# Performance work log

Hardware: AMD Instinct MI355X
Metric: run time of the kernel (lower is better)

The kernel has to match this reference:

```python
import jax, jax.numpy as jnp
import numpy as np

B, N = 32, 200000          # images, flattened candidates per image (anchors*classes)
NUM_CLASSES = 21           # VOC-style class count for the label-offset trick
CONF_THR = 0.05            # cfg.PRED_CONF_THR
NMS_THR = 0.5              # cfg.PRED_NMS_THR
TOPK = 500                 # cfg.PRED_SELECT_TOPK
KEEP_MAX = 100             # cfg.PRED_NMS_KEEP


def setup_inputs() -> dict:
    key = jax.random.key(0)
    k1, k2, k3, k4 = jax.random.split(key, 4)
    pscores = jax.random.uniform(k1, (B, N), dtype=jnp.float32)
    # well-formed ltrb boxes in [0,1]: right>left, bottom>top
    xy1 = jax.random.uniform(k2, (B, N, 2), dtype=jnp.float32) * 0.8
    wh = jax.random.uniform(k3, (B, N, 2), dtype=jnp.float32) * 0.2 + 0.01
    pboxes = jnp.concatenate([xy1, xy1 + wh], axis=-1)
    plabels = jax.random.randint(k4, (B, N), 0, NUM_CLASSES)
    return {"pscores": pscores, "pboxes": pboxes, "plabels": plabels}


def _box_iou(a, b):
    # a: [K,4], b: [K,4] ltrb -> [K,K] pairwise IoU (torchvision convention)
    lt = jnp.maximum(a[:, None, :2], b[None, :, :2])
    rb = jnp.minimum(a[:, None, 2:], b[None, :, 2:])
    wh = jnp.clip(rb - lt, 0.0)
    inter = wh[..., 0] * wh[..., 1]
    area_a = (a[:, 2] - a[:, 0]) * (a[:, 3] - a[:, 1])
    area_b = (b[:, 2] - b[:, 0]) * (b[:, 3] - b[:, 1])
    return inter / (area_a[:, None] + area_b[None, :] - inter)


def _greedy_nms(iou_mat, valid, thr):
    # candidates are pre-sorted by score descending (lax.top_k output order)
    K = valid.shape[0]
    idxs = jnp.arange(K)

    def body(keep, i):
        suppressed = jnp.any(keep & (iou_mat[i] > thr) & (idxs < i))
        k = valid[i] & (~suppressed)
        return keep.at[i].set(k), None

    keep, _ = jax.lax.scan(body, jnp.zeros((K,), dtype=bool), idxs)
    return keep


def reference(pscores, pboxes, plabels):
    # ---- threshold + top-k pre-selection (mask_pos AND mask_topk) ----
    scores_k, idx = jax.lax.top_k(pscores, TOPK)          # [B,K] sorted desc
    valid = scores_k > CONF_THR                           # equivalent to mask_pos & mask_topk
    bidx = jnp.arange(B)[:, None]
    boxes_k = pboxes[bidx, idx]                           # [B,K,4]
    labels_k = plabels[bidx, idx]                         # [B,K]

    # ---- multi-class NMS via label offset trick (batched_nms) ----
    max_coord = jnp.max(jnp.where(valid[..., None], boxes_k, 0.0), axis=(1, 2))  # [B]
    offsets = labels_k.astype(boxes_k.dtype) * (max_coord[:, None] + 1.0)
    boxes_nms = boxes_k + offsets[..., None]              # [B,K,4]

    iou = jax.vmap(_box_iou)(boxes_nms, boxes_nms)        # [B,K,K]
    keep = jax.vmap(lambda m, v: _greedy_nms(m, v, NMS_THR))(iou, valid)  # [B,K] bool

    # ---- keep[:num_max] per batch ----
    rank = jnp.cumsum(keep.astype(jnp.int32), axis=1)
    keep = keep & (rank <= KEEP_MAX)

    # compact kept entries to front (jnp.argsort is stable -> score order preserved), pad to KEEP_MAX
    order = jnp.argsort(jnp.where(keep, 0, 1), axis=1)[:, :KEEP_MAX]       # [B,KEEP]
    out_valid = jnp.take_along_axis(keep, order, axis=1)                    # [B,KEEP]
    boxes2 = jnp.take_along_axis(boxes_k, order[..., None], axis=1) * out_valid[..., None]
    scores2 = jnp.take_along_axis(scores_k, order, axis=1) * out_valid
    labels2 = jnp.where(out_valid, jnp.take_along_axis(labels_k, order, axis=1), -1)
    ids_batch2 = jnp.where(out_valid, jnp.arange(B)[:, None], -1)
    return ids_batch2, boxes2, labels2, scores2, out_valid
```

## Files before the change

kernel.cpp:

```cpp
#include <hip/hip_runtime.h>
#include <stdint.h>

#pragma clang fp contract(off)

#define BB 32
#define NN 200000
#define N4 50000
#define KK 500
#define KEEPN 100
#define CONF 0.05f
#define NMSTHR 0.5f
#define SLICES 8
#define SLICE_F4 6250
#define LBINS 8192
#define LSHIFT 19
#define LOCAL_CAP 2048
#define OUT_CAP 576
#define M_CAP (SLICES * OUT_CAP)

typedef unsigned long long u64;


__device__ __forceinline__ unsigned int ordkey(float s) {
    unsigned int u = __float_as_uint(s);
    return (u & 0x80000000u) ? ~u : (u | 0x80000000u);
}

__global__ __launch_bounds__(1024) void select_kernel(const float4* __restrict__ ps4,
                                                      u64* __restrict__ cand,
                                                      unsigned int* __restrict__ cnts) {
    __shared__ unsigned int hist[LBINS];
    __shared__ u64 keys[LOCAL_CAP];
    __shared__ unsigned int h[256];
    __shared__ unsigned int wsum[16];
    __shared__ u64 s_prefix;
    __shared__ unsigned int s_t13, s_region, s_cntgt;
    __shared__ int s_lcnt, s_sc;

    const int b = blockIdx.y, x = blockIdx.x;
    const int tid = threadIdx.x, lane = tid & 63, wv = tid >> 6;
    const float4* p = ps4 + (size_t)b * N4 + (size_t)x * SLICE_F4;

    for (int i = tid; i < LBINS; i += 1024) hist[i] = 0;
    __syncthreads();
    for (int i = tid; i < SLICE_F4; i += 1024) {
        float4 v = p[i];
        atomicAdd(&hist[ordkey(v.x) >> LSHIFT], 1u);
        atomicAdd(&hist[ordkey(v.y) >> LSHIFT], 1u);
        atomicAdd(&hist[ordkey(v.z) >> LSHIFT], 1u);
        atomicAdd(&hist[ordkey(v.w) >> LSHIFT], 1u);
    }
    __syncthreads();

    unsigned int v8[8], tot = 0;
    for (int j = 0; j < 8; ++j) { v8[j] = hist[tid * 8 + j]; tot += v8[j]; }
    unsigned int sfx = tot;
    for (int off = 1; off < 64; off <<= 1) {
        unsigned int t2 = __shfl_down(sfx, off);
        sfx += (lane + off < 64) ? t2 : 0u;
    }
    if (lane == 0) wsum[wv] = sfx;
    __syncthreads();
    unsigned int wafter = 0;
    for (int w2 = wv + 1; w2 < 16; ++w2) wafter += wsum[w2];
    unsigned int sn = wafter + (sfx - tot);
    for (int j = 7; j >= 0; --j) {
        unsigned int s = sn + v8[j];
        if (s >= (unsigned)KK && sn < (unsigned)KK) s_t13 = (unsigned)(tid * 8 + j);
        sn = s;
    }
    if (tid == 0) s_lcnt = 0;
    __syncthreads();

    const unsigned int t13 = s_t13;
    const int ebase = x * (SLICE_F4 * 4);
    for (int i = tid; i < SLICE_F4; i += 1024) {
        float4 v = p[i];
        int n = ebase + (i << 2);
        unsigned int u;
        u = ordkey(v.x); if ((u >> LSHIFT) >= t13) { int pos = atomicAdd(&s_lcnt, 1);
            if (pos < LOCAL_CAP) keys[pos] = ((u64)u << 32) | (unsigned int)(~(unsigned int)(n)); }
        u = ordkey(v.y); if ((u >> LSHIFT) >= t13) { int pos = atomicAdd(&s_lcnt, 1);
            if (pos < LOCAL_CAP) keys[pos] = ((u64)u << 32) | (unsigned int)(~(unsigned int)(n + 1)); }
        u = ordkey(v.z); if ((u >> LSHIFT) >= t13) { int pos = atomicAdd(&s_lcnt, 1);
            if (pos < LOCAL_CAP) keys[pos] = ((u64)u << 32) | (unsigned int)(~(unsigned int)(n + 2)); }
        u = ordkey(v.w); if ((u >> LSHIFT) >= t13) { int pos = atomicAdd(&s_lcnt, 1);
            if (pos < LOCAL_CAP) keys[pos] = ((u64)u << 32) | (unsigned int)(~(unsigned int)(n + 3)); }
    }
    __syncthreads();
    int m = s_lcnt; if (m > LOCAL_CAP) m = LOCAL_CAP;

    u64 thr; int seln;
    if (m <= OUT_CAP) {
        thr = 0ULL; seln = m;
    } else {
        if (tid == 0) { s_prefix = 0ULL; s_cntgt = 0u; }
        __syncthreads();
        int shift = 56;
        for (; shift >= 0; shift -= 8) {
            if (tid < 256) h[tid] = 0u;
            __syncthreads();
            u64 pref = s_prefix;
            unsigned int cg = s_cntgt;
            for (int i = tid; i < m; i += 1024) {
                u64 k = keys[i];
                bool match = (shift == 56) || ((k >> (shift + 8)) == pref);
                if (match) atomicAdd(&h[(unsigned int)((k >> shift) & 0xFF)], 1u);
            }
            __syncthreads();
            if (wv == 0) {
                unsigned int b4[4]; unsigned int lt = 0;
                for (int j = 0; j < 4; ++j) { b4[j] = h[lane * 4 + j]; lt += b4[j]; }
                unsigned int sx = lt;
                for (int off = 1; off < 64; off <<= 1) {
                    unsigned int t2 = __shfl_down(sx, off);
                    sx += (lane + off < 64) ? t2 : 0u;
                }
                unsigned int after = sx - lt;
                unsigned int target = (unsigned)KK - cg;
                unsigned int sn2 = after;
                for (int j = 3; j >= 0; --j) {
                    unsigned int s = sn2 + b4[j];
                    if (s >= target && sn2 < target) {
                        unsigned int bin = (unsigned)(lane * 4 + j);
                        s_region = b4[j];
                        s_cntgt = cg + sn2;
                        s_prefix = (shift == 56) ? (u64)bin : ((pref << 8) | (u64)bin);
                    }
                    sn2 = s;
                }
            }
            __syncthreads();
            if (s_cntgt + s_region <= (unsigned)OUT_CAP) break;
        }
        if (shift < 0) shift = 0;
        thr = s_prefix << shift;
        seln = (int)(s_cntgt + s_region);
    }
    (void)seln;

    if (tid == 0) s_sc = 0;
    __syncthreads();
    u64* outslice = cand + (size_t)(b * SLICES + x) * OUT_CAP;
    for (int r0 = 0; r0 < LOCAL_CAP / 1024; ++r0) {
        int i = tid + r0 * 1024;
        u64 k = (i < m) ? keys[i] : 0ULL;
        bool pq = (i < m) && (k >= thr);
        u64 mb = __ballot(pq);
        int pre = __popcll(mb & ((1ULL << lane) - 1ULL));
        int tt = __popcll(mb);
        int base = 0;
        if (lane == 0 && tt > 0) base = atomicAdd(&s_sc, tt);
        base = __shfl(base, 0);
        if (pq && base + pre < OUT_CAP) outslice[base + pre] = k;
    }
    __syncthreads();
    if (tid == 0) {
        int c = s_sc; if (c > OUT_CAP) c = OUT_CAP;
        cnts[b * SLICES + x] = (unsigned)c;
    }
}

__global__ __launch_bounds__(1024) void final_kernel(const float* __restrict__ pboxes,
                                                     const int* __restrict__ plabels,
                                                     const u64* __restrict__ cand,
                                                     const unsigned int* __restrict__ cnts,
                                                     float* __restrict__ out) {
    __shared__ u64 kbuf[M_CAP];
    __shared__ u64 sel[OUT_CAP];
    __shared__ float sboxes[KK * 4];
    __shared__ float sscore[KK];
    __shared__ int slabel[KK];
    __shared__ int clist[KK];
    __shared__ unsigned int h[256];
    __shared__ int ccnt[21], coff[22], cfill[21];
    __shared__ u64 validw[8];
    __shared__ int kept[KEEPN];
    __shared__ float wred[16];
    __shared__ int soff[SLICES + 1];
    __shared__ u64 s_prefix;
    __shared__ unsigned int s_region, s_cntgt;
    __shared__ int s_sc, s_nk;
    __shared__ float s_maxc;

    const int b = blockIdx.x;
    const int tid = threadIdx.x;
    const int lane = tid & 63;
    const int wv = tid >> 6;

    if (tid == 0) {
        int acc = 0;
        for (int s = 0; s < SLICES; ++s) {
            soff[s] = acc;
            int c = (int)cnts[b * SLICES + s];
            if (c > OUT_CAP) c = OUT_CAP;
            acc += c;
        }
        soff[SLICES] = acc;
    }
    __syncthreads();
    int m = soff[SLICES];
    for (int s = 0; s < SLICES; ++s) {
        int off = soff[s], len = soff[s + 1] - off;
        const u64* src = cand + (size_t)(b * SLICES + s) * OUT_CAP;
        for (int i = tid; i < len; i += 1024) kbuf[off + i] = src[i];
    }
    __syncthreads();

    u64 thr; int seln;
    if (m <= OUT_CAP) {
        thr = 0ULL; seln = m;
    } else {
        if (tid == 0) { s_prefix = 0ULL; s_cntgt = 0u; }
        __syncthreads();
        int shift = 56;
        for (; shift >= 0; shift -= 8) {
            if (tid < 256) h[tid] = 0u;
            __syncthreads();
            u64 pref = s_prefix;
            unsigned int cg = s_cntgt;
            for (int i = tid; i < m; i += 1024) {
                u64 k = kbuf[i];
                bool match = (shift == 56) || ((k >> (shift + 8)) == pref);
                if (match) atomicAdd(&h[(unsigned int)((k >> shift) & 0xFF)], 1u);
            }
            __syncthreads();
            if (wv == 0) {
                unsigned int b4[4]; unsigned int lt = 0;
                for (int j = 0; j < 4; ++j) { b4[j] = h[lane * 4 + j]; lt += b4[j]; }
                unsigned int sx = lt;
                for (int off = 1; off < 64; off <<= 1) {
                    unsigned int t2 = __shfl_down(sx, off);
                    sx += (lane + off < 64) ? t2 : 0u;
                }
                unsigned int after = sx - lt;
                unsigned int target = (unsigned)KK - cg;
                unsigned int sn2 = after;
                for (int j = 3; j >= 0; --j) {
                    unsigned int s = sn2 + b4[j];
                    if (s >= target && sn2 < target) {
                        unsigned int bin = (unsigned)(lane * 4 + j);
                        s_region = b4[j];
                        s_cntgt = cg + sn2;
                        s_prefix = (shift == 56) ? (u64)bin : ((pref << 8) | (u64)bin);
                    }
                    sn2 = s;
                }
            }
            __syncthreads();
            if (s_cntgt + s_region <= (unsigned)OUT_CAP) break;
        }
        if (shift < 0) shift = 0;
        thr = s_prefix << shift;
        seln = (int)(s_cntgt + s_region);
    }

    if (tid == 0) s_sc = 0;
    __syncthreads();
    for (int r0 = 0; r0 < (M_CAP + 1023) / 1024; ++r0) {
        int i = tid + r0 * 1024;
        u64 k = (i < m) ? kbuf[i] : 0ULL;
        bool pq = (i < m) && (k >= thr);
        u64 mb = __ballot(pq);
        int pre = __popcll(mb & ((1ULL << lane) - 1ULL));
        int tt = __popcll(mb);
        int base = 0;
        if (lane == 0 && tt > 0) base = atomicAdd(&s_sc, tt);
        base = __shfl(base, 0);
        if (pq) sel[base + pre] = k;
    }
    __syncthreads();

    u64 myk = (tid < seln) ? sel[tid] : 0ULL;
    int r = 0;
    if ((tid & ~63) < seln) {
        for (int base = 0; base < seln; base += 64) {
            int i2 = base + lane;
            u64 other = (i2 < seln) ? sel[i2] : 0ULL;
            unsigned int olo = (unsigned int)other, ohi = (unsigned int)(other >> 32);
            int lim = seln - base; if (lim > 64) lim = 64;
            for (int t2 = 0; t2 < lim; ++t2) {
                unsigned int blo = (unsigned int)__builtin_amdgcn_readlane((int)olo, t2);
                unsigned int bhi = (unsigned int)__builtin_amdgcn_readlane((int)ohi, t2);
                u64 o = ((u64)bhi << 32) | (u64)blo;
                r += (o > myk) ? 1 : 0;
            }
        }
    }
    __syncthreads();
    if (tid < seln && r < KK) sel[r] = myk;
    __syncthreads();

    float sc = -1.0f;
    if (tid < KK) {
        u64 key = sel[tid];
        unsigned int lo = (unsigned int)key;
        unsigned int hi = (unsigned int)(key >> 32);
        int idx = (int)(~lo);
        unsigned int bits = (hi & 0x80000000u) ? (hi & 0x7FFFFFFFu) : ~hi;
        sc = __uint_as_float(bits);
        sscore[tid] = sc;
        const float4 bx = *(const float4*)(pboxes + (((size_t)b * NN + (size_t)idx) << 2));
        sboxes[tid * 4 + 0] = bx.x; sboxes[tid * 4 + 1] = bx.y;
        sboxes[tid * 4 + 2] = bx.z; sboxes[tid * 4 + 3] = bx.w;
        slabel[tid] = plabels[(size_t)b * NN + idx];
    }
    __syncthreads();

    bool vq = (tid < KK) && (sc > CONF);
    u64 bm = __ballot(vq);
    if (lane == 0 && wv < 8) validw[wv] = bm;
    float lm = vq ? fmaxf(fmaxf(sboxes[tid * 4 + 0], sboxes[tid * 4 + 1]),
                          fmaxf(sboxes[tid * 4 + 2], sboxes[tid * 4 + 3])) : 0.0f;
    for (int off = 32; off > 0; off >>= 1) lm = fmaxf(lm, __shfl_down(lm, off));
    if (lane == 0) wred[wv] = lm;
    __syncthreads();
    if (tid < 64) {
        float x = (tid < 16) ? wred[tid] : 0.0f;
        for (int off = 8; off > 0; off >>= 1) x = fmaxf(x, __shfl_down(x, off));
        if (tid == 0) s_maxc = x;
    }
    if (tid < 21) { ccnt[tid] = 0; cfill[tid] = 0; }
    __syncthreads();
    if (tid < KK) atomicAdd(&ccnt[slabel[tid]], 1);
    __syncthreads();
    if (tid == 0) {
        int acc = 0;
        for (int c = 0; c < 21; ++c) { coff[c] = acc; acc += ccnt[c]; }
        coff[21] = acc;
    }
    __syncthreads();
    if (tid < KK) {
        int c = slabel[tid];
        int pos = atomicAdd(&cfill[c], 1);
        clist[coff[c] + pos] = tid;
    }
    for (int i = tid; i < KK * 8; i += 1024) kbuf[i] = 0ULL;
    __syncthreads();

    float ap1 = s_maxc + 1.0f;
    if (tid < KK) {
        int c = slabel[tid];
        int n = ccnt[c], base0 = coff[c];
        float aoff = (float)c * ap1;
        float a0 = sboxes[tid * 4 + 0] + aoff, a1 = sboxes[tid * 4 + 1] + aoff;
        float a2 = sboxes[tid * 4 + 2] + aoff, a3 = sboxes[tid * 4 + 3] + aoff;
        float areaA = (a2 - a0) * (a3 - a1);
        for (int q = 0; q < n; ++q) {
            int j = clist[base0 + q];
            float b0 = sboxes[j * 4 + 0] + aoff, b1f = sboxes[j * 4 + 1] + aoff;
            float b2f = sboxes[j * 4 + 2] + aoff, b3f = sboxes[j * 4 + 3] + aoff;
            float lt0 = fmaxf(a0, b0), lt1 = fmaxf(a1, b1f);
            float rb0 = fminf(a2, b2f), rb1 = fminf(a3, b3f);
            float ww = fmaxf(rb0 - lt0, 0.0f), hh = fmaxf(rb1 - lt1, 0.0f);
            float inter = ww * hh;
            float areaB = (b2f - b0) * (b3f - b1f);
            float iou = inter / (areaA + areaB - inter);
            if (iou > NMSTHR) kbuf[tid * 8 + (j >> 6)] |= (1ULL << (j & 63));
        }
    }
    __syncthreads();

    if (tid < 64) {
        u64 remv = 0ULL;
        u64 vw_reg = (lane < 8) ? validw[lane] : 0ULL;
        int nk = 0;
        for (int i = 0; i < KK && nk < KEEPN; ++i) {
            int w = i >> 6, bpos = i & 63;
            u64 rw = __shfl(remv, w);
            u64 vv = __shfl(vw_reg, w);
            bool alive = (((vv >> bpos) & 1ULL) != 0ULL) && (((rw >> bpos) & 1ULL) == 0ULL);
            if (alive) {
                if (lane == 0) kept[nk] = i;
                u64 roww = (lane < 8) ? kbuf[i * 8 + lane] : 0ULL;
                remv |= roww;
                nk++;
            }
        }
        if (lane == 0) s_nk = nk;
    }
    __syncthreads();

    if (tid < KEEPN) {
        const int O_BOX = BB * KEEPN;
        const int O_LAB = BB * KEEPN * 5;
        const int O_SCO = BB * KEEPN * 6;
        const int O_VAL = BB * KEEPN * 7;
        bool q = tid < s_nk;
        int i = q ? kept[tid] : 0;
        int g = b * KEEPN + tid;
        out[g]                 = q ? (float)b : -1.0f;
        out[O_BOX + g * 4 + 0] = q ? sboxes[i * 4 + 0] : 0.0f;
        out[O_BOX + g * 4 + 1] = q ? sboxes[i * 4 + 1] : 0.0f;
        out[O_BOX + g * 4 + 2] = q ? sboxes[i * 4 + 2] : 0.0f;
        out[O_BOX + g * 4 + 3] = q ? sboxes[i * 4 + 3] : 0.0f;
        out[O_LAB + g]         = q ? (float)slabel[i] : -1.0f;
        out[O_SCO + g]         = q ? sscore[i] : 0.0f;
        out[O_VAL + g]         = q ? 1.0f : 0.0f;
    }
}

extern "C" void kernel_launch(void* const* d_in, const int* in_sizes, int n_in,
                              void* d_out, int out_size, void* d_ws, size_t ws_size,
                              hipStream_t stream) {
    const float* pscores = (const float*)d_in[0];
    const float* pboxes  = (const float*)d_in[1];
    const int*   plabels = (const int*)d_in[2];
    float* out = (float*)d_out;

    uint8_t* ws = (uint8_t*)d_ws;
    u64*          cand = (u64*)(ws + 0);
    unsigned int* cnts = (unsigned int*)(ws + 1179648);

    select_kernel<<<dim3(SLICES, BB), 1024, 0, stream>>>((const float4*)pscores, cand, cnts);
    final_kernel<<<BB, 1024, 0, stream>>>(pboxes, plabels, cand, cnts, out);
}
```

Measured before the change: 227.0 us.

## Aggregate candidate atomics per wave, skip radix passes, faster greedy NMS scan

The select kernel now compacts candidates with one ballot-based atomic per wave instead of one LDS atomic per element. Both radix-select loops first compute the min and max keys and start at the first byte where they differ, so leading passes that cannot split the keys are skipped. The greedy NMS loop jumps straight to the next alive candidate with ballot and ctz instead of visiting all 500 indices. The final kernel also drops to 512 threads, and OUT_CAP shrinks to 512, which reduces the per-slice candidate buffers and the workspace offsets.

```diff
diff --git a/kernel.cpp b/kernel.cpp
--- a/kernel.cpp
+++ b/kernel.cpp
@@ -15,7 +15,7 @@
 #define LBINS 8192
 #define LSHIFT 19
 #define LOCAL_CAP 2048
-#define OUT_CAP 576
+#define OUT_CAP 512
 #define M_CAP (SLICES * OUT_CAP)
 
 typedef unsigned long long u64;
@@ -33,7 +33,8 @@
     __shared__ u64 keys[LOCAL_CAP];
     __shared__ unsigned int h[256];
     __shared__ unsigned int wsum[16];
-    __shared__ u64 s_prefix;
+    __shared__ u64 wmn[16], wmx[16];
+    __shared__ u64 s_prefix, s_mn, s_mx;
     __shared__ unsigned int s_t13, s_region, s_cntgt;
     __shared__ int s_lcnt, s_sc;
 
@@ -77,26 +78,57 @@
     for (int i = tid; i < SLICE_F4; i += 1024) {
         float4 v = p[i];
         int n = ebase + (i << 2);
-        unsigned int u;
-        u = ordkey(v.x); if ((u >> LSHIFT) >= t13) { int pos = atomicAdd(&s_lcnt, 1);
-            if (pos < LOCAL_CAP) keys[pos] = ((u64)u << 32) | (unsigned int)(~(unsigned int)(n)); }
-        u = ordkey(v.y); if ((u >> LSHIFT) >= t13) { int pos = atomicAdd(&s_lcnt, 1);
-            if (pos < LOCAL_CAP) keys[pos] = ((u64)u << 32) | (unsigned int)(~(unsigned int)(n + 1)); }
-        u = ordkey(v.z); if ((u >> LSHIFT) >= t13) { int pos = atomicAdd(&s_lcnt, 1);
-            if (pos < LOCAL_CAP) keys[pos] = ((u64)u << 32) | (unsigned int)(~(unsigned int)(n + 2)); }
-        u = ordkey(v.w); if ((u >> LSHIFT) >= t13) { int pos = atomicAdd(&s_lcnt, 1);
-            if (pos < LOCAL_CAP) keys[pos] = ((u64)u << 32) | (unsigned int)(~(unsigned int)(n + 3)); }
+        float cmp[4] = {v.x, v.y, v.z, v.w};
+        #pragma unroll
+        for (int c = 0; c < 4; ++c) {
+            unsigned int u = ordkey(cmp[c]);
+            bool pq = (u >> LSHIFT) >= t13;
+            u64 mb = __ballot(pq);
+            if (mb) {
+                int pre = __popcll(mb & ((1ULL << lane) - 1ULL));
+                int tt = __popcll(mb);
+                int base = 0;
+                if (lane == 0) base = atomicAdd(&s_lcnt, tt);
+                base = __shfl(base, 0);
+                int pos = base + pre;
+                if (pq && pos < LOCAL_CAP)
+                    keys[pos] = ((u64)u << 32) | (unsigned int)(~(unsigned int)(n + c));
+            }
+        }
     }
     __syncthreads();
     int m = s_lcnt; if (m > LOCAL_CAP) m = LOCAL_CAP;
 
-    u64 thr; int seln;
+    u64 thr;
     if (m <= OUT_CAP) {
-        thr = 0ULL; seln = m;
+        thr = 0ULL;
     } else {
-        if (tid == 0) { s_prefix = 0ULL; s_cntgt = 0u; }
-        __syncthreads();
-        int shift = 56;
+        u64 mn = ~0ULL, mx = 0ULL;
+        for (int i = tid; i < m; i += 1024) {
+            u64 k = keys[i];
+            mn = (k < mn) ? k : mn; mx = (k > mx) ? k : mx;
+        }
+        for (int off = 32; off > 0; off >>= 1) {
+            u64 a = __shfl_down(mn, off), c = __shfl_down(mx, off);
+            if (lane + off < 64) { mn = (a < mn) ? a : mn; mx = (c > mx) ? c : mx; }
+        }
+        if (lane == 0) { wmn[wv] = mn; wmx[wv] = mx; }
+        __syncthreads();
+        if (tid == 0) {
+            u64 a = ~0ULL, c = 0ULL;
+            for (int w2 = 0; w2 < 16; ++w2) {
+                a = (wmn[w2] < a) ? wmn[w2] : a;
+                c = (wmx[w2] > c) ? wmx[w2] : c;
+            }
+            s_mn = a; s_mx = c; s_cntgt = 0u;
+        }
+        __syncthreads();
+        u64 dx = s_mn ^ s_mx;
+        int hb = 63 - __builtin_clzll(dx | 1ULL);
+        int s0 = (hb >> 3) << 3;
+        if (tid == 0) s_prefix = (s0 == 56) ? 0ULL : (s_mx >> (s0 + 8));
+        __syncthreads();
+        int shift = s0;
         for (; shift >= 0; shift -= 8) {
             if (tid < 256) h[tid] = 0u;
             __syncthreads();
@@ -104,7 +136,7 @@
             unsigned int cg = s_cntgt;
             for (int i = tid; i < m; i += 1024) {
                 u64 k = keys[i];
-                bool match = (shift == 56) || ((k >> (shift + 8)) == pref);
+                bool match = (shift == s0) || ((k >> (shift + 8)) == pref);
                 if (match) atomicAdd(&h[(unsigned int)((k >> shift) & 0xFF)], 1u);
             }
             __syncthreads();
@@ -135,9 +167,7 @@
         }
         if (shift < 0) shift = 0;
         thr = s_prefix << shift;
-        seln = (int)(s_cntgt + s_region);
-    }
-    (void)seln;
+    }
 
     if (tid == 0) s_sc = 0;
     __syncthreads();
@@ -161,11 +191,11 @@
     }
 }
 
-__global__ __launch_bounds__(1024) void final_kernel(const float* __restrict__ pboxes,
-                                                     const int* __restrict__ plabels,
-                                                     const u64* __restrict__ cand,
-                                                     const unsigned int* __restrict__ cnts,
-                                                     float* __restrict__ out) {
+__global__ __launch_bounds__(512) void final_kernel(const float* __restrict__ pboxes,
+                                                    const int* __restrict__ plabels,
+                                                    const u64* __restrict__ cand,
+                                                    const unsigned int* __restrict__ cnts,
+                                                    float* __restrict__ out) {
     __shared__ u64 kbuf[M_CAP];
     __shared__ u64 sel[OUT_CAP];
     __shared__ float sboxes[KK * 4];
@@ -176,9 +206,10 @@
     __shared__ int ccnt[21], coff[22], cfill[21];
     __shared__ u64 validw[8];
     __shared__ int kept[KEEPN];
-    __shared__ float wred[16];
+    __shared__ float wred[8];
+    __shared__ u64 wmn[8], wmx[8];
     __shared__ int soff[SLICES + 1];
-    __shared__ u64 s_prefix;
+    __shared__ u64 s_prefix, s_mn, s_mx;
     __shared__ unsigned int s_region, s_cntgt;
     __shared__ int s_sc, s_nk;
     __shared__ float s_maxc;
@@ -203,7 +234,7 @@
     for (int s = 0; s < SLICES; ++s) {
         int off = soff[s], len = soff[s + 1] - off;
         const u64* src = cand + (size_t)(b * SLICES + s) * OUT_CAP;
-        for (int i = tid; i < len; i += 1024) kbuf[off + i] = src[i];
+        for (int i = tid; i < len; i += 512) kbuf[off + i] = src[i];
     }
     __syncthreads();
 
@@ -211,17 +242,40 @@
     if (m <= OUT_CAP) {
         thr = 0ULL; seln = m;
     } else {
-        if (tid == 0) { s_prefix = 0ULL; s_cntgt = 0u; }
-        __syncthreads();
-        int shift = 56;
+        u64 mn = ~0ULL, mx = 0ULL;
+        for (int i = tid; i < m; i += 512) {
+            u64 k = kbuf[i];
+            mn = (k < mn) ? k : mn; mx = (k > mx) ? k : mx;
+        }
+        for (int off = 32; off > 0; off >>= 1) {
+            u64 a = __shfl_down(mn, off), c = __shfl_down(mx, off);
+            if (lane + off < 64) { mn = (a < mn) ? a : mn; mx = (c > mx) ? c : mx; }
+        }
+        if (lane == 0) { wmn[wv] = mn; wmx[wv] = mx; }
+        __syncthreads();
+        if (tid == 0) {
+            u64 a = ~0ULL, c = 0ULL;
+            for (int w2 = 0; w2 < 8; ++w2) {
+                a = (wmn[w2] < a) ? wmn[w2] : a;
+                c = (wmx[w2] > c) ? wmx[w2] : c;
+            }
+            s_mn = a; s_mx = c; s_cntgt = 0u;
+        }
+        __syncthreads();
+        u64 dx = s_mn ^ s_mx;
+        int hb = 63 - __builtin_clzll(dx | 1ULL);
+        int s0 = (hb >> 3) << 3;
+        if (tid == 0) s_prefix = (s0 == 56) ? 0ULL : (s_mx >> (s0 + 8));
+        __syncthreads();
+        int shift = s0;
         for (; shift >= 0; shift -= 8) {
             if (tid < 256) h[tid] = 0u;
             __syncthreads();
             u64 pref = s_prefix;
             unsigned int cg = s_cntgt;
-            for (int i = tid; i < m; i += 1024) {
+            for (int i = tid; i < m; i += 512) {
                 u64 k = kbuf[i];
-                bool match = (shift == 56) || ((k >> (shift + 8)) == pref);
+                bool match = (shift == s0) || ((k >> (shift + 8)) == pref);
                 if (match) atomicAdd(&h[(unsigned int)((k >> shift) & 0xFF)], 1u);
             }
             __syncthreads();
@@ -257,8 +311,8 @@
 
     if (tid == 0) s_sc = 0;
     __syncthreads();
-    for (int r0 = 0; r0 < (M_CAP + 1023) / 1024; ++r0) {
-        int i = tid + r0 * 1024;
+    for (int r0 = 0; r0 < (M_CAP + 511) / 512; ++r0) {
+        int i = tid + r0 * 512;
         u64 k = (i < m) ? kbuf[i] : 0ULL;
         bool pq = (i < m) && (k >= thr);
         u64 mb = __ballot(pq);
@@ -309,15 +363,15 @@
 
     bool vq = (tid < KK) && (sc > CONF);
     u64 bm = __ballot(vq);
-    if (lane == 0 && wv < 8) validw[wv] = bm;
+    if (lane == 0) validw[wv] = bm;
     float lm = vq ? fmaxf(fmaxf(sboxes[tid * 4 + 0], sboxes[tid * 4 + 1]),
                           fmaxf(sboxes[tid * 4 + 2], sboxes[tid * 4 + 3])) : 0.0f;
     for (int off = 32; off > 0; off >>= 1) lm = fmaxf(lm, __shfl_down(lm, off));
     if (lane == 0) wred[wv] = lm;
     __syncthreads();
     if (tid < 64) {
-        float x = (tid < 16) ? wred[tid] : 0.0f;
-        for (int off = 8; off > 0; off >>= 1) x = fmaxf(x, __shfl_down(x, off));
+        float x = (tid < 8) ? wred[tid] : 0.0f;
+        for (int off = 4; off > 0; off >>= 1) x = fmaxf(x, __shfl_down(x, off));
         if (tid == 0) s_maxc = x;
     }
     if (tid < 21) { ccnt[tid] = 0; cfill[tid] = 0; }
@@ -335,7 +389,7 @@
         int pos = atomicAdd(&cfill[c], 1);
         clist[coff[c] + pos] = tid;
     }
-    for (int i = tid; i < KK * 8; i += 1024) kbuf[i] = 0ULL;
+    for (int i = tid; i < KK * 8; i += 512) kbuf[i] = 0ULL;
     __syncthreads();
 
     float ap1 = s_maxc + 1.0f;
@@ -362,20 +416,20 @@
     __syncthreads();
 
     if (tid < 64) {
-        u64 remv = 0ULL;
-        u64 vw_reg = (lane < 8) ? validw[lane] : 0ULL;
+        u64 alive = (lane < 8) ? validw[lane] : 0ULL;
         int nk = 0;
-        for (int i = 0; i < KK && nk < KEEPN; ++i) {
-            int w = i >> 6, bpos = i & 63;
-            u64 rw = __shfl(remv, w);
-            u64 vv = __shfl(vw_reg, w);
-            bool alive = (((vv >> bpos) & 1ULL) != 0ULL) && (((rw >> bpos) & 1ULL) == 0ULL);
-            if (alive) {
-                if (lane == 0) kept[nk] = i;
-                u64 roww = (lane < 8) ? kbuf[i * 8 + lane] : 0ULL;
-                remv |= roww;
-                nk++;
-            }
+        while (nk < KEEPN) {
+            u64 wm = __ballot(alive != 0ULL);
+            if (wm == 0ULL) break;
+            int f = __builtin_ctzll(wm);
+            int bp = (alive != 0ULL) ? __builtin_ctzll(alive) : 0;
+            int i = __shfl((lane << 6) + bp, f);
+            if (lane == 0) kept[nk] = i;
+            nk++;
+            if (nk >= KEEPN) break;
+            u64 row = (lane < 8) ? kbuf[i * 8 + lane] : 0ULL;
+            if (lane == (i >> 6)) row |= (1ULL << (i & 63));
+            alive &= ~row;
         }
         if (lane == 0) s_nk = nk;
     }
@@ -410,8 +464,8 @@
 
     uint8_t* ws = (uint8_t*)d_ws;
     u64*          cand = (u64*)(ws + 0);
-    unsigned int* cnts = (unsigned int*)(ws + 1179648);
+    unsigned int* cnts = (unsigned int*)(ws + 1048576);
 
     select_kernel<<<dim3(SLICES, BB), 1024, 0, stream>>>((const float4*)pscores, cand, cnts);
-    final_kernel<<<BB, 1024, 0, stream>>>(pboxes, plabels, cand, cnts, out);
+    final_kernel<<<BB, 512, 0, stream>>>(pboxes, plabels, cand, cnts, out);
 }
```

Result: slower. 233.3 us (+2.8%).
